# Kernel optimization log

Hardware: AMD Instinct MI355X
Metric: run time of the kernel (lower is better)

Reference implementation:

```python
import jax, jax.numpy as jnp
import numpy as np
from jax import lax

# ConvTranspose2d(stride=1, padding=p) == conv with spatially-flipped, in/out-swapped
# weight and padding k-1-p per side. Here k=3, p=1 -> conv padding (1,1).
K = 3
P = 1
_CONV_PAD = K - 1 - P  # = 1

def _rconv(a, w):
    # a: [N,C,H,Wf] real, w: [O,I,kH,kW]
    return lax.conv_general_dilated(
        a, w, window_strides=(1, 1),
        padding=[(_CONV_PAD, _CONV_PAD), (_CONV_PAD, _CONV_PAD)],
        dimension_numbers=("NCHW", "OIHW", "NCHW"))


def setup_inputs() -> dict:
    key = jax.random.key(0)
    k1, k2, k3, k4, k5 = jax.random.split(key, 5)
    N, C_IN, C_OUT, H, W = 8, 16, 16, 512, 512
    x = jax.random.normal(k1, (N, C_IN, H, W), dtype=jnp.float32)
    # torch ConvTranspose2d weight layout: (in, out, kH, kW), complex64 split into re/im
    scale = 1.0 / np.sqrt(C_IN * K * K)
    w_real = jax.random.normal(k2, (C_IN, C_OUT, K, K), dtype=jnp.float32) * scale
    w_imag = jax.random.normal(k3, (C_IN, C_OUT, K, K), dtype=jnp.float32) * scale
    b_real = jax.random.normal(k4, (C_OUT,), dtype=jnp.float32) * scale
    b_imag = jax.random.normal(k5, (C_OUT,), dtype=jnp.float32) * scale
    return {"x": x, "w_real": w_real, "w_imag": w_imag, "b_real": b_real, "b_imag": b_imag}


def reference(x, w_real, w_imag, b_real, b_imag):
    # rfftn over last two dims (norm='backward')
    X = jnp.fft.rfftn(x, axes=(-2, -1), norm="backward")  # [N,C,H,W//2+1] complex64
    Xr, Xi = jnp.real(X), jnp.imag(X)
    # convert transpose-conv weight to equivalent conv weight: flip spatial, swap in/out
    wr = jnp.transpose(jnp.flip(w_real, axis=(-2, -1)), (1, 0, 2, 3))
    wi = jnp.transpose(jnp.flip(w_imag, axis=(-2, -1)), (1, 0, 2, 3))
    # complex conv via real/imag decomposition
    Yr = _rconv(Xr, wr) - _rconv(Xi, wi) + b_real[:, None, None]
    Yi = _rconv(Xr, wi) + _rconv(Xi, wr) + b_imag[:, None, None]
    Y = lax.complex(Yr, Yi)
    # irfftn with no explicit s: last dim -> 2*(Wf-1) = W
    return jnp.fft.irfftn(Y, axes=(-2, -1), norm="backward")
```

## Files before the change

### kernel.cpp

```cpp
#include <hip/hip_runtime.h>
#include <math.h>

#define PI_F 3.14159265358979323846f

#define FI(i) ((i) + ((i) >> 4))
#define CSTRIDE 544

__device__ inline float2 cmulf(float2 a, float2 b) {
    return make_float2(a.x * b.x - a.y * b.y, a.x * b.y + a.y * b.x);
}
__device__ inline float2 cadd(float2 a, float2 b) { return make_float2(a.x + b.x, a.y + b.y); }
__device__ inline float2 csub(float2 a, float2 b) { return make_float2(a.x - b.x, a.y - b.y); }

__device__ inline void cmac(float2& a, float2 w, float2 v) {
    a.x = fmaf(w.x, v.x, a.x);
    a.x = fmaf(-w.y, v.y, a.x);
    a.y = fmaf(w.x, v.y, a.y);
    a.y = fmaf(w.y, v.x, a.y);
}

__device__ inline void build_tbl128(float2* tbl, int tid) {
    if (tid < 128) {
        float ang = -2.0f * PI_F * (float)tid * (1.0f / 512.0f);
        tbl[tid] = make_float2(cosf(ang), sinf(ang));
    }
}

template <int NCOLS>
__device__ inline float2* fft512_r4(float2* a, float2* b, const float2* tbl, int tid, bool inv) {
    const int bf = tid & 127;
    const int cp = tid >> 7;
#pragma unroll
    for (int st = 0; st < 4; ++st) {
        const int slog = 2 * st;
        const int s = 1 << slog;
        const int p = bf >> slog;
        const int q = bf & (s - 1);
        float2 w1 = tbl[p << slog];
        if (inv) w1.y = -w1.y;
        const float2 w2 = cmulf(w1, w1);
        const float2 w3 = cmulf(w2, w1);
        const int i0 = bf;
        const int ob = q + (p << (slog + 2));
#pragma unroll
        for (int t = 0; t < NCOLS / 2; ++t) {
            const int cc = cp + 2 * t;
            const float2* ac = a + cc * CSTRIDE;
            float2* bc = b + cc * CSTRIDE;
            float2 A = ac[FI(i0)];
            float2 B = ac[FI(i0 + 128)];
            float2 C = ac[FI(i0 + 256)];
            float2 D = ac[FI(i0 + 384)];
            float2 apc = cadd(A, C), amc = csub(A, C);
            float2 bpd = cadd(B, D), bmd = csub(B, D);
            float2 jb = make_float2(-bmd.y, bmd.x);
            if (inv) { jb.x = -jb.x; jb.y = -jb.y; }
            bc[FI(ob)]           = cadd(apc, bpd);
            bc[FI(ob + s)]       = cmulf(csub(amc, jb), w1);
            bc[FI(ob + 2 * s)]   = cmulf(csub(apc, bpd), w2);
            bc[FI(ob + 3 * s)]   = cmulf(cadd(amc, jb), w3);
        }
        __syncthreads();
        float2* tmp = a; a = b; b = tmp;
    }
    {
#pragma unroll
        for (int cc = 0; cc < NCOLS; ++cc) {
            const float2* ac = a + cc * CSTRIDE;
            float2* bc = b + cc * CSTRIDE;
            float2 A = ac[FI(tid)];
            float2 B = ac[FI(tid + 256)];
            bc[FI(tid)]       = cadd(A, B);
            bc[FI(tid + 256)] = csub(A, B);
        }
        __syncthreads();
        float2* tmp = a; a = b; b = tmp;
    }
    return a;
}

__global__ __launch_bounds__(256) void k_row_rfft(const float* __restrict__ x,
                                                  float2* __restrict__ G) {
    __shared__ float2 b0[4 * CSTRIDE], b1[4 * CSTRIDE], tbl[128];
    int tid = threadIdx.x;
    int nc = blockIdx.x >> 7;
    int h0 = (blockIdx.x & 127) * 4;
    build_tbl128(tbl, tid);
    const float4* xr = (const float4*)(x + ((size_t)nc * 512 + h0) * 512);
#pragma unroll
    for (int j = 0; j < 2; ++j) {
        int t4 = tid + 256 * j;
        float4 v = xr[t4];
        int e = t4 * 4;
        int k = e >> 9, i = e & 511;
        float2* dst = b0 + k * CSTRIDE + FI(i);
        dst[0] = make_float2(v.x, 0.0f);
        dst[1] = make_float2(v.y, 0.0f);
        dst[2] = make_float2(v.z, 0.0f);
        dst[3] = make_float2(v.w, 0.0f);
    }
    __syncthreads();
    float2* res = fft512_r4<4>(b0, b1, tbl, tid, false);
#pragma unroll
    for (int k = 0; k < 4; ++k) {
        float2* g = G + ((size_t)(nc * 512 + h0 + k)) * 257;
        g[tid] = res[k * CSTRIDE + FI(tid)];
        if (tid == 0) g[256] = res[k * CSTRIDE + FI(256)];
    }
}

__global__ __launch_bounds__(256) void k_col_fft(const float2* __restrict__ G,
                                                 float2* __restrict__ XT) {
    __shared__ float2 b0[4 * CSTRIDE], b1[4 * CSTRIDE], tbl[128];
    int tid = threadIdx.x;
    int nc = blockIdx.x / 65;
    int v0 = (blockIdx.x % 65) * 4;
    build_tbl128(tbl, tid);
#pragma unroll
    for (int i = 0; i < 8; ++i) {
        int e = tid + 256 * i;
        int k = e & 3, h = e >> 2;
        int v = v0 + k;
        float2 val = make_float2(0.0f, 0.0f);
        if (v < 257) val = G[((size_t)nc * 512 + h) * 257 + v];
        b0[k * CSTRIDE + FI(h)] = val;
    }
    __syncthreads();
    float2* res = fft512_r4<4>(b0, b1, tbl, tid, false);
#pragma unroll
    for (int k = 0; k < 4; ++k) {
        int v = v0 + k;
        if (v < 257) {
            float2* dst = XT + ((size_t)nc * 257 + v) * 512;
            dst[tid]       = res[k * CSTRIDE + FI(tid)];
            dst[tid + 256] = res[k * CSTRIDE + FI(tid + 256)];
        }
    }
}

__global__ __launch_bounds__(256, 6) void k_conv(const float2* __restrict__ XT,
                                                 float2* __restrict__ YT,
                                                 const float* __restrict__ wr,
                                                 const float* __restrict__ wi,
                                                 const float* __restrict__ br,
                                                 const float* __restrict__ bi) {
    __shared__ float2 Xs[16 * 3 * 66];
    int tid = threadIdx.x;
    int bid = blockIdx.x;
    int ut = bid & 7;
    int rest = bid >> 3;
    int v = rest % 257;
    int n = rest / 257;
    int u0 = ut * 64;

    for (int l = tid; l < 3168; l += 256) {
        int c = l / 198;
        int rem = l - c * 198;
        int dv = rem / 66;
        int uu = rem - dv * 66;
        int vg = v - 1 + dv;
        int ug = u0 - 1 + uu;
        float2 val = make_float2(0.0f, 0.0f);
        if (vg >= 0 && vg < 257 && ug >= 0 && ug < 512)
            val = XT[(((size_t)n * 16 + c) * 257 + vg) * 512 + ug];
        Xs[l] = val;
    }
    __syncthreads();

    int lane = tid & 63;
    int wv = __builtin_amdgcn_readfirstlane(tid >> 6);
    int o0 = wv * 4;

    float2 acc[4];
#pragma unroll
    for (int oo = 0; oo < 4; ++oo)
        acc[oo] = make_float2(br[o0 + oo], bi[o0 + oo]);

    for (int c = 0; c < 16; ++c) {
        float2 xv[3][3];
#pragma unroll
        for (int dv = 0; dv < 3; ++dv) {
            const float2* row = &Xs[(c * 3 + dv) * 66];
            xv[dv][0] = row[lane];
            xv[dv][1] = row[lane + 1];
            xv[dv][2] = row[lane + 2];
        }
#pragma unroll
        for (int oo = 0; oo < 4; ++oo) {
            const float* wrp = wr + ((size_t)(c * 16 + o0 + oo)) * 9;
            const float* wip = wi + ((size_t)(c * 16 + o0 + oo)) * 9;
            float wre[9], wim[9];
#pragma unroll
            for (int t = 0; t < 9; ++t) { wre[t] = wrp[t]; wim[t] = wip[t]; }
#pragma unroll
            for (int dv = 0; dv < 3; ++dv) {
                int kw = 2 - dv;
#pragma unroll
                for (int kh = 0; kh < 3; ++kh) {
                    int t = kh * 3 + kw;
                    float2 w = make_float2(wre[t], wim[t]);
                    cmac(acc[oo], w, xv[dv][2 - kh]);
                }
            }
        }
    }

#pragma unroll
    for (int oo = 0; oo < 4; ++oo) {
        YT[(((size_t)n * 16 + o0 + oo) * 257 + v) * 512 + u0 + lane] = acc[oo];
    }
}

__global__ __launch_bounds__(256) void k_col_ifft(const float2* __restrict__ YT,
                                                  float2* __restrict__ ZT) {
    __shared__ float2 b0[4 * CSTRIDE], b1[4 * CSTRIDE], tbl[128];
    int tid = threadIdx.x;
    int no = blockIdx.x / 65;
    int v0 = (blockIdx.x % 65) * 4;
    build_tbl128(tbl, tid);
#pragma unroll
    for (int k = 0; k < 4; ++k) {
        int v = v0 + k;
        const float2* src = YT + ((size_t)no * 257 + (v < 257 ? v : 256)) * 512;
        b0[k * CSTRIDE + FI(tid)]       = src[tid];
        b0[k * CSTRIDE + FI(tid + 256)] = src[tid + 256];
    }
    __syncthreads();
    float2* res = fft512_r4<4>(b0, b1, tbl, tid, true);
    const float sc = 1.0f / 512.0f;
#pragma unroll
    for (int k = 0; k < 4; ++k) {
        int v = v0 + k;
        if (v < 257) {
            float2* dst = ZT + ((size_t)no * 257 + v) * 512;
            float2 r0 = res[k * CSTRIDE + FI(tid)];
            float2 r1 = res[k * CSTRIDE + FI(tid + 256)];
            dst[tid]       = make_float2(r0.x * sc, r0.y * sc);
            dst[tid + 256] = make_float2(r1.x * sc, r1.y * sc);
        }
    }
}

__global__ __launch_bounds__(256) void k_row_irfft(const float2* __restrict__ ZT,
                                                   float* __restrict__ out) {
    __shared__ float2 b0[4 * CSTRIDE], b1[4 * CSTRIDE], tbl[128];
    int tid = threadIdx.x;
    int no = blockIdx.x >> 7;
    int h0 = (blockIdx.x & 127) * 4;
    build_tbl128(tbl, tid);
#pragma unroll
    for (int i = 0; i < 5; ++i) {
        int e = tid + 256 * i;
        if (e < 1028) {
            int k = e & 3, vv = e >> 2;
            float2 val = ZT[((size_t)no * 257 + vv) * 512 + h0 + k];
            if (vv == 0 || vv == 256) val.y = 0.0f;
            b0[k * CSTRIDE + FI(vv)] = val;
        }
    }
    __syncthreads();
#pragma unroll
    for (int i = 0; i < 4; ++i) {
        int e = tid + 256 * i;
        if (e < 1020) {
            int k = e & 3, vv = 257 + (e >> 2);
            float2 s = b0[k * CSTRIDE + FI(512 - vv)];
            b0[k * CSTRIDE + FI(vv)] = make_float2(s.x, -s.y);
        }
    }
    __syncthreads();
    float2* res = fft512_r4<4>(b0, b1, tbl, tid, true);
    const float sc = 1.0f / 512.0f;
#pragma unroll
    for (int k = 0; k < 4; ++k) {
        float* dst = out + ((size_t)no * 512 + h0 + k) * 512;
        dst[tid]       = res[k * CSTRIDE + FI(tid)].x * sc;
        dst[tid + 256] = res[k * CSTRIDE + FI(tid + 256)].x * sc;
    }
}

extern "C" void kernel_launch(void* const* d_in, const int* in_sizes, int n_in,
                              void* d_out, int out_size, void* d_ws, size_t ws_size,
                              hipStream_t stream) {
    const float* x  = (const float*)d_in[0];
    const float* wr = (const float*)d_in[1];
    const float* wi = (const float*)d_in[2];
    const float* br = (const float*)d_in[3];
    const float* bi = (const float*)d_in[4];
    float* out = (float*)d_out;

    const size_t bufElems = (size_t)128 * 257 * 512;
    float2* A = (float2*)d_ws;
    float2* B = A + bufElems;

    k_row_rfft<<<128 * 128, 256, 0, stream>>>(x, A);
    k_col_fft<<<128 * 65, 256, 0, stream>>>(A, B);
    k_conv<<<8 * 257 * 8, 256, 0, stream>>>(B, A, wr, wi, br, bi);
    k_col_ifft<<<128 * 65, 256, 0, stream>>>(A, B);
    k_row_irfft<<<128 * 128, 256, 0, stream>>>(B, out);
}
```

Measured before the change: 721.3 us.

## Use 3-multiply complex MAC in conv and remap blocks across XCDs

The complex convolution now uses the Gauss three-multiplication trick. It keeps P=wr·xr, Q=wi·xi and R=(wr+wi)(xr+xi), so the real and imaginary outputs are formed from 3 FMAs per tap instead of 4. The summed weights are computed by block 0 of the first kernel into the output buffer as scratch, which is later overwritten. The column-FFT and row-iFFT kernels also remap block indices so neighbouring work lands on the same XCD, aiming at better L2 locality. The trade-off is one extra weight load stream per tap plus the added adds, and a cross-kernel dependency on the scratch sums.

Measured after the change: 714.3 us. About the same (-1.0%).

```diff
diff --git a/kernel.cpp b/kernel.cpp
--- a/kernel.cpp
+++ b/kernel.cpp
@@ -12,11 +12,8 @@
 __device__ inline float2 cadd(float2 a, float2 b) { return make_float2(a.x + b.x, a.y + b.y); }
 __device__ inline float2 csub(float2 a, float2 b) { return make_float2(a.x - b.x, a.y - b.y); }
 
-__device__ inline void cmac(float2& a, float2 w, float2 v) {
-    a.x = fmaf(w.x, v.x, a.x);
-    a.x = fmaf(-w.y, v.y, a.x);
-    a.y = fmaf(w.x, v.y, a.y);
-    a.y = fmaf(w.y, v.x, a.y);
+__device__ inline int xcd_remap(int bid, int q) {
+    return (bid & 7) * q + (bid >> 3);
 }
 
 __device__ inline void build_tbl128(float2* tbl, int tid) {
@@ -80,11 +77,17 @@
 }
 
 __global__ __launch_bounds__(256) void k_row_rfft(const float* __restrict__ x,
-                                                  float2* __restrict__ G) {
+                                                  float2* __restrict__ G,
+                                                  const float* __restrict__ wr,
+                                                  const float* __restrict__ wi,
+                                                  float* __restrict__ wsum) {
     __shared__ float2 b0[4 * CSTRIDE], b1[4 * CSTRIDE], tbl[128];
     int tid = threadIdx.x;
     int nc = blockIdx.x >> 7;
     int h0 = (blockIdx.x & 127) * 4;
+    if (blockIdx.x == 0) {
+        for (int l = tid; l < 2304; l += 256) wsum[l] = wr[l] + wi[l];
+    }
     build_tbl128(tbl, tid);
     const float4* xr = (const float4*)(x + ((size_t)nc * 512 + h0) * 512);
 #pragma unroll
@@ -113,8 +116,9 @@
                                                  float2* __restrict__ XT) {
     __shared__ float2 b0[4 * CSTRIDE], b1[4 * CSTRIDE], tbl[128];
     int tid = threadIdx.x;
-    int nc = blockIdx.x / 65;
-    int v0 = (blockIdx.x % 65) * 4;
+    int l = xcd_remap(blockIdx.x, 1040);
+    int nc = l / 65;
+    int v0 = (l % 65) * 4;
     build_tbl128(tbl, tid);
 #pragma unroll
     for (int i = 0; i < 8; ++i) {
@@ -142,6 +146,7 @@
                                                  float2* __restrict__ YT,
                                                  const float* __restrict__ wr,
                                                  const float* __restrict__ wi,
+                                                 const float* __restrict__ wsm,
                                                  const float* __restrict__ br,
                                                  const float* __restrict__ bi) {
     __shared__ float2 Xs[16 * 3 * 66];
@@ -171,35 +176,43 @@
     int wv = __builtin_amdgcn_readfirstlane(tid >> 6);
     int o0 = wv * 4;
 
-    float2 acc[4];
-#pragma unroll
-    for (int oo = 0; oo < 4; ++oo)
-        acc[oo] = make_float2(br[o0 + oo], bi[o0 + oo]);
+    float accP[4] = {0.f, 0.f, 0.f, 0.f};
+    float accQ[4] = {0.f, 0.f, 0.f, 0.f};
+    float accR[4] = {0.f, 0.f, 0.f, 0.f};
 
     for (int c = 0; c < 16; ++c) {
         float2 xv[3][3];
+        float sx[3][3];
 #pragma unroll
         for (int dv = 0; dv < 3; ++dv) {
             const float2* row = &Xs[(c * 3 + dv) * 66];
             xv[dv][0] = row[lane];
             xv[dv][1] = row[lane + 1];
             xv[dv][2] = row[lane + 2];
+            sx[dv][0] = xv[dv][0].x + xv[dv][0].y;
+            sx[dv][1] = xv[dv][1].x + xv[dv][1].y;
+            sx[dv][2] = xv[dv][2].x + xv[dv][2].y;
         }
 #pragma unroll
         for (int oo = 0; oo < 4; ++oo) {
-            const float* wrp = wr + ((size_t)(c * 16 + o0 + oo)) * 9;
-            const float* wip = wi + ((size_t)(c * 16 + o0 + oo)) * 9;
-            float wre[9], wim[9];
-#pragma unroll
-            for (int t = 0; t < 9; ++t) { wre[t] = wrp[t]; wim[t] = wip[t]; }
+            const float* wrp = wr  + ((size_t)(c * 16 + o0 + oo)) * 9;
+            const float* wip = wi  + ((size_t)(c * 16 + o0 + oo)) * 9;
+            const float* wsp = wsm + ((size_t)(c * 16 + o0 + oo)) * 9;
+            float wre[9], wim[9], wsu[9];
+#pragma unroll
+            for (int t = 0; t < 9; ++t) {
+                wre[t] = wrp[t]; wim[t] = wip[t]; wsu[t] = wsp[t];
+            }
 #pragma unroll
             for (int dv = 0; dv < 3; ++dv) {
                 int kw = 2 - dv;
 #pragma unroll
                 for (int kh = 0; kh < 3; ++kh) {
                     int t = kh * 3 + kw;
-                    float2 w = make_float2(wre[t], wim[t]);
-                    cmac(acc[oo], w, xv[dv][2 - kh]);
+                    int xj = 2 - kh;
+                    accP[oo] = fmaf(wre[t], xv[dv][xj].x, accP[oo]);
+                    accQ[oo] = fmaf(wim[t], xv[dv][xj].y, accQ[oo]);
+                    accR[oo] = fmaf(wsu[t], sx[dv][xj],  accR[oo]);
                 }
             }
         }
@@ -207,7 +220,10 @@
 
 #pragma unroll
     for (int oo = 0; oo < 4; ++oo) {
-        YT[(((size_t)n * 16 + o0 + oo) * 257 + v) * 512 + u0 + lane] = acc[oo];
+        float re = accP[oo] - accQ[oo] + br[o0 + oo];
+        float im = accR[oo] - accP[oo] - accQ[oo] + bi[o0 + oo];
+        YT[(((size_t)n * 16 + o0 + oo) * 257 + v) * 512 + u0 + lane] =
+            make_float2(re, im);
     }
 }
 
@@ -245,8 +261,9 @@
                                                    float* __restrict__ out) {
     __shared__ float2 b0[4 * CSTRIDE], b1[4 * CSTRIDE], tbl[128];
     int tid = threadIdx.x;
-    int no = blockIdx.x >> 7;
-    int h0 = (blockIdx.x & 127) * 4;
+    int l = xcd_remap(blockIdx.x, 2048);
+    int no = l >> 7;
+    int h0 = (l & 127) * 4;
     build_tbl128(tbl, tid);
 #pragma unroll
     for (int i = 0; i < 5; ++i) {
@@ -292,10 +309,11 @@
     const size_t bufElems = (size_t)128 * 257 * 512;
     float2* A = (float2*)d_ws;
     float2* B = A + bufElems;
-
-    k_row_rfft<<<128 * 128, 256, 0, stream>>>(x, A);
+    float* wsum = out;
+
+    k_row_rfft<<<128 * 128, 256, 0, stream>>>(x, A, wr, wi, wsum);
     k_col_fft<<<128 * 65, 256, 0, stream>>>(A, B);
-    k_conv<<<8 * 257 * 8, 256, 0, stream>>>(B, A, wr, wi, br, bi);
+    k_conv<<<8 * 257 * 8, 256, 0, stream>>>(B, A, wr, wi, wsum, br, bi);
     k_col_ifft<<<128 * 65, 256, 0, stream>>>(A, B);
     k_row_irfft<<<128 * 128, 256, 0, stream>>>(B, out);
 }
```

## Transpose intermediate FFT layouts for coalesced access and remap blocks across XCDs

Applied to the files above, without the earlier changes.

Row rFFT now writes its output frequency-major, so the column FFT reads contiguous rows instead of gathering strided elements. Likewise, the column iFFT writes row-major, so the row irFFT reads contiguous rows. This moves the strided traffic to the writes, which are partially vectorized as float4. Block indices are also remapped so consecutive logical blocks land on the same XCD, which is meant to improve L2 locality, at the risk of uneven XCD load.

After: 719.1 us. About the same (-0.3%).

```diff
diff --git a/kernel.cpp b/kernel.cpp
--- a/kernel.cpp
+++ b/kernel.cpp
@@ -17,6 +17,10 @@
     a.x = fmaf(-w.y, v.y, a.x);
     a.y = fmaf(w.x, v.y, a.y);
     a.y = fmaf(w.y, v.x, a.y);
+}
+
+__device__ inline int xcd_remap(int bid, int q) {
+    return (bid & 7) * q + (bid >> 3);
 }
 
 __device__ inline void build_tbl128(float2* tbl, int tid) {
@@ -80,11 +84,12 @@
 }
 
 __global__ __launch_bounds__(256) void k_row_rfft(const float* __restrict__ x,
-                                                  float2* __restrict__ G) {
+                                                  float2* __restrict__ GT) {
     __shared__ float2 b0[4 * CSTRIDE], b1[4 * CSTRIDE], tbl[128];
     int tid = threadIdx.x;
-    int nc = blockIdx.x >> 7;
-    int h0 = (blockIdx.x & 127) * 4;
+    int l = xcd_remap(blockIdx.x, 2048);
+    int nc = l >> 7;
+    int h0 = (l & 127) * 4;
     build_tbl128(tbl, tid);
     const float4* xr = (const float4*)(x + ((size_t)nc * 512 + h0) * 512);
 #pragma unroll
@@ -101,28 +106,43 @@
     }
     __syncthreads();
     float2* res = fft512_r4<4>(b0, b1, tbl, tid, false);
-#pragma unroll
-    for (int k = 0; k < 4; ++k) {
-        float2* g = G + ((size_t)(nc * 512 + h0 + k)) * 257;
-        g[tid] = res[k * CSTRIDE + FI(tid)];
-        if (tid == 0) g[256] = res[k * CSTRIDE + FI(256)];
-    }
-}
-
-__global__ __launch_bounds__(256) void k_col_fft(const float2* __restrict__ G,
+    {
+        float2* g = GT + ((size_t)nc * 257 + tid) * 512 + h0;
+        float4* g4 = (float4*)g;
+        float2 r0 = res[0 * CSTRIDE + FI(tid)];
+        float2 r1 = res[1 * CSTRIDE + FI(tid)];
+        float2 r2 = res[2 * CSTRIDE + FI(tid)];
+        float2 r3 = res[3 * CSTRIDE + FI(tid)];
+        g4[0] = make_float4(r0.x, r0.y, r1.x, r1.y);
+        g4[1] = make_float4(r2.x, r2.y, r3.x, r3.y);
+        if (tid == 0) {
+            float2* gn = GT + ((size_t)nc * 257 + 256) * 512 + h0;
+            float4* gn4 = (float4*)gn;
+            float2 s0 = res[0 * CSTRIDE + FI(256)];
+            float2 s1 = res[1 * CSTRIDE + FI(256)];
+            float2 s2 = res[2 * CSTRIDE + FI(256)];
+            float2 s3 = res[3 * CSTRIDE + FI(256)];
+            gn4[0] = make_float4(s0.x, s0.y, s1.x, s1.y);
+            gn4[1] = make_float4(s2.x, s2.y, s3.x, s3.y);
+        }
+    }
+}
+
+__global__ __launch_bounds__(256) void k_col_fft(const float2* __restrict__ GT,
                                                  float2* __restrict__ XT) {
     __shared__ float2 b0[4 * CSTRIDE], b1[4 * CSTRIDE], tbl[128];
     int tid = threadIdx.x;
-    int nc = blockIdx.x / 65;
-    int v0 = (blockIdx.x % 65) * 4;
+    int l = xcd_remap(blockIdx.x, 1040);
+    int nc = l / 65;
+    int v0 = (l % 65) * 4;
     build_tbl128(tbl, tid);
 #pragma unroll
     for (int i = 0; i < 8; ++i) {
         int e = tid + 256 * i;
-        int k = e & 3, h = e >> 2;
+        int k = e >> 9, h = e & 511;
         int v = v0 + k;
         float2 val = make_float2(0.0f, 0.0f);
-        if (v < 257) val = G[((size_t)nc * 512 + h) * 257 + v];
+        if (v < 257) val = GT[((size_t)nc * 257 + v) * 512 + h];
         b0[k * CSTRIDE + FI(h)] = val;
     }
     __syncthreads();
@@ -212,11 +232,12 @@
 }
 
 __global__ __launch_bounds__(256) void k_col_ifft(const float2* __restrict__ YT,
-                                                  float2* __restrict__ ZT) {
+                                                  float2* __restrict__ ZTT) {
     __shared__ float2 b0[4 * CSTRIDE], b1[4 * CSTRIDE], tbl[128];
     int tid = threadIdx.x;
-    int no = blockIdx.x / 65;
-    int v0 = (blockIdx.x % 65) * 4;
+    int l = xcd_remap(blockIdx.x, 1040);
+    int no = l / 65;
+    int v0 = (l % 65) * 4;
     build_tbl128(tbl, tid);
 #pragma unroll
     for (int k = 0; k < 4; ++k) {
@@ -228,34 +249,37 @@
     __syncthreads();
     float2* res = fft512_r4<4>(b0, b1, tbl, tid, true);
     const float sc = 1.0f / 512.0f;
-#pragma unroll
-    for (int k = 0; k < 4; ++k) {
-        int v = v0 + k;
-        if (v < 257) {
-            float2* dst = ZT + ((size_t)no * 257 + v) * 512;
+    float2* d0 = ZTT + ((size_t)no * 512 + tid) * 257 + v0;
+    float2* d1 = ZTT + ((size_t)no * 512 + tid + 256) * 257 + v0;
+#pragma unroll
+    for (int k = 0; k < 4; ++k) {
+        if (v0 + k < 257) {
             float2 r0 = res[k * CSTRIDE + FI(tid)];
             float2 r1 = res[k * CSTRIDE + FI(tid + 256)];
-            dst[tid]       = make_float2(r0.x * sc, r0.y * sc);
-            dst[tid + 256] = make_float2(r1.x * sc, r1.y * sc);
-        }
-    }
-}
-
-__global__ __launch_bounds__(256) void k_row_irfft(const float2* __restrict__ ZT,
+            d0[k] = make_float2(r0.x * sc, r0.y * sc);
+            d1[k] = make_float2(r1.x * sc, r1.y * sc);
+        }
+    }
+}
+
+__global__ __launch_bounds__(256) void k_row_irfft(const float2* __restrict__ ZTT,
                                                    float* __restrict__ out) {
     __shared__ float2 b0[4 * CSTRIDE], b1[4 * CSTRIDE], tbl[128];
     int tid = threadIdx.x;
-    int no = blockIdx.x >> 7;
-    int h0 = (blockIdx.x & 127) * 4;
+    int l = xcd_remap(blockIdx.x, 2048);
+    int no = l >> 7;
+    int h0 = (l & 127) * 4;
     build_tbl128(tbl, tid);
 #pragma unroll
-    for (int i = 0; i < 5; ++i) {
-        int e = tid + 256 * i;
-        if (e < 1028) {
-            int k = e & 3, vv = e >> 2;
-            float2 val = ZT[((size_t)no * 257 + vv) * 512 + h0 + k];
-            if (vv == 0 || vv == 256) val.y = 0.0f;
-            b0[k * CSTRIDE + FI(vv)] = val;
+    for (int k = 0; k < 4; ++k) {
+        const float2* src = ZTT + ((size_t)no * 512 + h0 + k) * 257;
+        float2 val = src[tid];
+        if (tid == 0) val.y = 0.0f;
+        b0[k * CSTRIDE + FI(tid)] = val;
+        if (tid == 0) {
+            float2 vn = src[256];
+            vn.y = 0.0f;
+            b0[k * CSTRIDE + FI(256)] = vn;
         }
     }
     __syncthreads();
```

## Compute two v-rows per conv block and remap blocks across XCDs

Applied to the files above, without the earlier changes.

The conv kernel now produces two adjacent frequency rows per block. Its shared tile grows from 3 to 4 halo rows, and each weight load feeds two accumulators, which cuts halo reload traffic and weight-load overhead per output. The launch-bounds occupancy hint drops from 6 to 4 to leave room for the extra registers. The column FFT and row irfft kernels remap block indices so that consecutive logical blocks land on the same XCD, aiming for better L2 locality. This costs some occupancy and adds a boundary guard for the odd final row.

Measured after the change: 674.6 us. 1.07x faster.

```diff
diff --git a/kernel.cpp b/kernel.cpp
--- a/kernel.cpp
+++ b/kernel.cpp
@@ -17,6 +17,10 @@
     a.x = fmaf(-w.y, v.y, a.x);
     a.y = fmaf(w.x, v.y, a.y);
     a.y = fmaf(w.y, v.x, a.y);
+}
+
+__device__ inline int xcd_remap(int bid, int q) {
+    return (bid & 7) * q + (bid >> 3);
 }
 
 __device__ inline void build_tbl128(float2* tbl, int tid) {
@@ -113,8 +117,9 @@
                                                  float2* __restrict__ XT) {
     __shared__ float2 b0[4 * CSTRIDE], b1[4 * CSTRIDE], tbl[128];
     int tid = threadIdx.x;
-    int nc = blockIdx.x / 65;
-    int v0 = (blockIdx.x % 65) * 4;
+    int l = xcd_remap(blockIdx.x, 1040);
+    int nc = l / 65;
+    int v0 = (l % 65) * 4;
     build_tbl128(tbl, tid);
 #pragma unroll
     for (int i = 0; i < 8; ++i) {
@@ -138,27 +143,28 @@
     }
 }
 
-__global__ __launch_bounds__(256, 6) void k_conv(const float2* __restrict__ XT,
+__global__ __launch_bounds__(256, 4) void k_conv(const float2* __restrict__ XT,
                                                  float2* __restrict__ YT,
                                                  const float* __restrict__ wr,
                                                  const float* __restrict__ wi,
                                                  const float* __restrict__ br,
                                                  const float* __restrict__ bi) {
-    __shared__ float2 Xs[16 * 3 * 66];
+    __shared__ float2 Xs[16 * 4 * 66];
     int tid = threadIdx.x;
     int bid = blockIdx.x;
     int ut = bid & 7;
     int rest = bid >> 3;
-    int v = rest % 257;
-    int n = rest / 257;
+    int vt = rest % 129;
+    int n = rest / 129;
     int u0 = ut * 64;
-
-    for (int l = tid; l < 3168; l += 256) {
-        int c = l / 198;
-        int rem = l - c * 198;
-        int dv = rem / 66;
-        int uu = rem - dv * 66;
-        int vg = v - 1 + dv;
+    int v0 = vt * 2;
+
+    for (int l = tid; l < 4224; l += 256) {
+        int c = l / 264;
+        int rem = l - c * 264;
+        int dvr = rem / 66;
+        int uu = rem - dvr * 66;
+        int vg = v0 - 1 + dvr;
         int ug = u0 - 1 + uu;
         float2 val = make_float2(0.0f, 0.0f);
         if (vg >= 0 && vg < 257 && ug >= 0 && ug < 512)
@@ -171,19 +177,22 @@
     int wv = __builtin_amdgcn_readfirstlane(tid >> 6);
     int o0 = wv * 4;
 
-    float2 acc[4];
-#pragma unroll
-    for (int oo = 0; oo < 4; ++oo)
-        acc[oo] = make_float2(br[o0 + oo], bi[o0 + oo]);
+    float2 acc[2][4];
+#pragma unroll
+    for (int oo = 0; oo < 4; ++oo) {
+        float2 bv = make_float2(br[o0 + oo], bi[o0 + oo]);
+        acc[0][oo] = bv;
+        acc[1][oo] = bv;
+    }
 
     for (int c = 0; c < 16; ++c) {
-        float2 xv[3][3];
-#pragma unroll
-        for (int dv = 0; dv < 3; ++dv) {
-            const float2* row = &Xs[(c * 3 + dv) * 66];
-            xv[dv][0] = row[lane];
-            xv[dv][1] = row[lane + 1];
-            xv[dv][2] = row[lane + 2];
+        float2 xv[4][3];
+#pragma unroll
+        for (int dvr = 0; dvr < 4; ++dvr) {
+            const float2* row = &Xs[(c * 4 + dvr) * 66];
+            xv[dvr][0] = row[lane];
+            xv[dvr][1] = row[lane + 1];
+            xv[dvr][2] = row[lane + 2];
         }
 #pragma unroll
         for (int oo = 0; oo < 4; ++oo) {
@@ -193,13 +202,14 @@
 #pragma unroll
             for (int t = 0; t < 9; ++t) { wre[t] = wrp[t]; wim[t] = wip[t]; }
 #pragma unroll
-            for (int dv = 0; dv < 3; ++dv) {
-                int kw = 2 - dv;
+            for (int kw = 0; kw < 3; ++kw) {
 #pragma unroll
                 for (int kh = 0; kh < 3; ++kh) {
                     int t = kh * 3 + kw;
+                    int xj = 2 - kh;
                     float2 w = make_float2(wre[t], wim[t]);
-                    cmac(acc[oo], w, xv[dv][2 - kh]);
+                    cmac(acc[0][oo], w, xv[2 - kw][xj]);
+                    cmac(acc[1][oo], w, xv[3 - kw][xj]);
                 }
             }
         }
@@ -207,7 +217,13 @@
 
 #pragma unroll
     for (int oo = 0; oo < 4; ++oo) {
-        YT[(((size_t)n * 16 + o0 + oo) * 257 + v) * 512 + u0 + lane] = acc[oo];
+#pragma unroll
+        for (int vv = 0; vv < 2; ++vv) {
+            int v = v0 + vv;
+            if (v < 257)
+                YT[(((size_t)n * 16 + o0 + oo) * 257 + v) * 512 + u0 + lane] =
+                    acc[vv][oo];
+        }
     }
 }
 
@@ -245,8 +261,9 @@
                                                    float* __restrict__ out) {
     __shared__ float2 b0[4 * CSTRIDE], b1[4 * CSTRIDE], tbl[128];
     int tid = threadIdx.x;
-    int no = blockIdx.x >> 7;
-    int h0 = (blockIdx.x & 127) * 4;
+    int l = xcd_remap(blockIdx.x, 2048);
+    int no = l >> 7;
+    int h0 = (l & 127) * 4;
     build_tbl128(tbl, tid);
 #pragma unroll
     for (int i = 0; i < 5; ++i) {
@@ -295,7 +312,7 @@
 
     k_row_rfft<<<128 * 128, 256, 0, stream>>>(x, A);
     k_col_fft<<<128 * 65, 256, 0, stream>>>(A, B);
-    k_conv<<<8 * 257 * 8, 256, 0, stream>>>(B, A, wr, wi, br, bi);
+    k_conv<<<8 * 129 * 8, 256, 0, stream>>>(B, A, wr, wi, br, bi);
     k_col_ifft<<<128 * 65, 256, 0, stream>>>(A, B);
     k_row_irfft<<<128 * 128, 256, 0, stream>>>(B, out);
 }
```
